# Optimization experiments

Hardware: AMD Instinct MI355X
Metric: run time of the kernel (lower is better)

Reference implementation:

```python
import jax, jax.numpy as jnp
import numpy as np
from jax import lax

PAD_IDX = 0  # padding_index from init
B, T, E, H, V = 128, 24, 512, 512, 10000


def setup_inputs() -> dict:
    key = jax.random.key(0)
    ks = jax.random.split(key, 10)
    return {
        "images": jax.random.normal(ks[0], (B, H), jnp.float32),
        "captions": jax.random.randint(ks[1], (B, T), 0, V),
        "captions_length": jax.random.randint(ks[2], (B,), 1, T + 1),
        "W_emb": jax.random.normal(ks[3], (V, E), jnp.float32) * 0.02,
        "W_ih": jax.random.normal(ks[4], (4 * H, E), jnp.float32) * 0.02,
        "W_hh": jax.random.normal(ks[5], (4 * H, H), jnp.float32) * 0.02,
        "b_ih": jax.random.normal(ks[6], (4 * H,), jnp.float32) * 0.02,
        "b_hh": jax.random.normal(ks[7], (4 * H,), jnp.float32) * 0.02,
        "W_out": jax.random.normal(ks[8], (V, H), jnp.float32) * 0.02,
        "b_out": jax.random.normal(ks[9], (V,), jnp.float32) * 0.02,
    }


def reference(images, captions, captions_length, W_emb, W_ih, W_hh, b_ih, b_hh, W_out, b_out):
    # embedding with padding_idx: padding row forced to zero
    emb_table = W_emb.at[PAD_IDX].set(0.0)
    x = emb_table[captions]  # [B, T, E]
    bdim = images.shape[0]
    hdim = W_hh.shape[1]
    vocab = W_out.shape[0]
    bias = b_ih + b_hh

    def step(carry, xt):
        h, c = carry
        # PyTorch LSTMCell gate order: i, f, g, o
        gates = xt @ W_ih.T + h @ W_hh.T + bias  # [B, 4H]
        i, f, g, o = jnp.split(gates, 4, axis=-1)
        c = jax.nn.sigmoid(f) * c + jax.nn.sigmoid(i) * jnp.tanh(g)
        h = jax.nn.sigmoid(o) * jnp.tanh(c)
        logits = h @ W_out.T + b_out  # [B, V]
        return (h, c), logits

    c0 = jnp.zeros((bdim, hdim), images.dtype)
    _, ys = lax.scan(step, (images, c0), jnp.transpose(x, (1, 0, 2)))  # ys: [T, B, V]

    # deterministic <SOS>-like start output: one-hot at index 1, prepended at t=0
    start = jnp.zeros((vocab,), images.dtype).at[1].set(1.0)
    outputs = jnp.concatenate(
        [jnp.broadcast_to(start, (bdim, 1, vocab)), jnp.transpose(ys, (1, 0, 2))], axis=1
    )  # [B, T+1, V]
    return outputs, captions_length - 1
```

## Files before the change

### kernel.cpp

```cpp
#include <hip/hip_runtime.h>

constexpr int B_  = 128;
constexpr int T_  = 24;
constexpr int E_  = 512;
constexpr int H_  = 512;
constexpr int V_  = 10000;
constexpr int G4  = 2048;
constexpr int TP1 = 25;

typedef __attribute__((ext_vector_type(8))) short bf16x8;
typedef __attribute__((ext_vector_type(4))) short short4v;
typedef __attribute__((ext_vector_type(4))) float f32x4;

#define MFMA_16x16x32_BF16(a, b, c) __builtin_amdgcn_mfma_f32_16x16x32_bf16((a), (b), (c), 0, 0, 0)

__device__ inline unsigned short f2bf(float f) {
    unsigned int u = __float_as_uint(f);
    unsigned int r = (u + 0x7FFFu + ((u >> 16) & 1u)) >> 16;
    return (unsigned short)r;
}

__device__ inline void gl16(const unsigned short* g, unsigned short* l) {
    __builtin_amdgcn_global_load_lds(
        (const __attribute__((address_space(1))) unsigned int*)g,
        (__attribute__((address_space(3))) unsigned int*)l, 16, 0, 0);
}

__device__ inline int swz16(int row, int lq) {
    return (((row << 2) | lq) ^ (row & 7)) << 3;
}

__global__ __launch_bounds__(256) void k_cvt_all(const float* __restrict__ Wih,
                                                 const float* __restrict__ Whh,
                                                 const float* __restrict__ Wout,
                                                 const float* __restrict__ images,
                                                 unsigned short* __restrict__ dWih,
                                                 unsigned short* __restrict__ dWhh,
                                                 unsigned short* __restrict__ dWout,
                                                 unsigned short* __restrict__ dimg,
                                                 unsigned* __restrict__ flg) {
    int b = blockIdx.x;
    if (b == 0) flg[threadIdx.x * 32] = 0u;
    const float* src; unsigned short* dst; int i;
    if (b < 1024)      { src = Wih;    dst = dWih;  i = b * 256 + threadIdx.x; }
    else if (b < 2048) { src = Whh;    dst = dWhh;  i = (b - 1024) * 256 + threadIdx.x; }
    else if (b < 7048) { src = Wout;   dst = dWout; i = (b - 2048) * 256 + threadIdx.x; }
    else               { src = images; dst = dimg;  i = (b - 7048) * 256 + threadIdx.x; }
    float4 v = ((const float4*)src)[i];
    short4v o;
    o[0] = (short)f2bf(v.x); o[1] = (short)f2bf(v.y);
    o[2] = (short)f2bf(v.z); o[3] = (short)f2bf(v.w);
    ((short4v*)dst)[i] = o;
}

__global__ __launch_bounds__(256) void k_embed(const float* __restrict__ Wemb,
                                               const int* __restrict__ captions,
                                               unsigned short* __restrict__ Xemb) {
    int i = blockIdx.x * 256 + threadIdx.x;
    if (i >= 3072 * 128) return;
    int row = i >> 7;
    int k4  = i & 127;
    int b = row & 127, t = row >> 7;
    int tok = captions[b * T_ + t];
    short4v o = {0, 0, 0, 0};
    if (tok > 0 && tok < V_) {
        float4 v = ((const float4*)(Wemb + (long)tok * E_))[k4];
        o[0] = (short)f2bf(v.x); o[1] = (short)f2bf(v.y);
        o[2] = (short)f2bf(v.z); o[3] = (short)f2bf(v.w);
    }
    ((short4v*)Xemb)[(long)row * 128 + k4] = o;
}

__global__ __launch_bounds__(256) void k_start(float* __restrict__ out,
                                               const int* __restrict__ cap_len) {
    int idx = blockIdx.x * 256 + threadIdx.x;
    constexpr int Q = V_ / 4;
    if (idx < B_ * Q) {
        int b = idx / Q;
        int q = idx - b * Q;
        float4 zero = {0.f, 0.f, 0.f, 0.f};
        float4 one1 = {0.f, 1.f, 0.f, 0.f};
        ((float4*)out)[(long)b * (TP1 * Q) + q] = (q == 0) ? one1 : zero;
    }
    if (idx < B_) {
        out[(size_t)B_ * TP1 * V_ + idx] = (float)(cap_len[idx] - 1);
    }
}

__global__ __launch_bounds__(256) void k_pregemm(const unsigned short* __restrict__ Xemb,
                                                 const unsigned short* __restrict__ Wih,
                                                 const float* __restrict__ bih,
                                                 const float* __restrict__ bhh,
                                                 float* __restrict__ P) {
    __shared__ unsigned short ldsA[2][4096];
    __shared__ unsigned short ldsB[2][4096];
    int bid = blockIdx.x;
    int xcd = bid & 7;
    int q   = bid >> 3;
    int MI  = xcd * 3 + (q % 3);
    int NI  = q / 3;
    int i    = threadIdx.x;
    int w = i >> 6, lane = i & 63;
    int lm = lane & 15, lq = lane >> 4;
    int wr = w >> 1, wc = w & 1;

    int mm0 = ((i >> 2) & 7) ^ ((i >> 4) & 1);
    int li  = i ^ mm0;
    const unsigned short* gA = Xemb + (size_t)(MI * 128 + (li >> 2)) * 512 + (li & 3) * 8;
    const unsigned short* gB = Wih  + (size_t)(NI * 128 + (li >> 2)) * 512 + (li & 3) * 8;
    unsigned short* lA = &ldsA[0][0] + i * 8;
    unsigned short* lB = &ldsB[0][0] + i * 8;

    auto stage = [&](int buf, int ks) {
        int go = ks * 32;
        gl16(gA + go,            lA + buf * 4096);
        gl16(gA + go + 64 * 512, lA + buf * 4096 + 2048);
        gl16(gB + go,            lB + buf * 4096);
        gl16(gB + go + 64 * 512, lB + buf * 4096 + 2048);
    };

    f32x4 acc[4][4] = {};
    stage(0, 0);
    for (int ksi = 0; ksi < 16; ksi++) {
        int cur = ksi & 1;
        if (ksi < 15) stage(cur ^ 1, ksi + 1);
        __syncthreads();
        bf16x8 af[4], bfr[4];
        #pragma unroll
        for (int mi = 0; mi < 4; mi++)
            af[mi] = *(const bf16x8*)&ldsA[cur][swz16(wr * 64 + mi * 16 + lm, lq)];
        #pragma unroll
        for (int ni = 0; ni < 4; ni++)
            bfr[ni] = *(const bf16x8*)&ldsB[cur][swz16(wc * 64 + ni * 16 + lm, lq)];
        #pragma unroll
        for (int mi = 0; mi < 4; mi++)
            #pragma unroll
            for (int ni = 0; ni < 4; ni++)
                acc[mi][ni] = MFMA_16x16x32_BF16(af[mi], bfr[ni], acc[mi][ni]);
        __syncthreads();
    }

    float bias[4];
    #pragma unroll
    for (int ni = 0; ni < 4; ni++) {
        int n = NI * 128 + wc * 64 + ni * 16 + lm;
        bias[ni] = bih[n] + bhh[n];
    }
    #pragma unroll
    for (int mi = 0; mi < 4; mi++) {
        #pragma unroll
        for (int r = 0; r < 4; r++) {
            int m = MI * 128 + wr * 64 + mi * 16 + lq * 4 + r;
            #pragma unroll
            for (int ni = 0; ni < 4; ni++) {
                int n = NI * 128 + wc * 64 + ni * 16 + lm;
                P[(size_t)m * G4 + n] = acc[mi][ni][r] + bias[ni];
            }
        }
    }
}

__global__ __launch_bounds__(256, 1) void k_lstm(const float* __restrict__ P,
                                                 const unsigned short* __restrict__ h0,
                                                 unsigned* __restrict__ hx0,
                                                 unsigned* __restrict__ hx1,
                                                 unsigned short* __restrict__ Hall,
                                                 const unsigned short* __restrict__ Whh,
                                                 unsigned* __restrict__ flg) {
    __shared__ float part[16][4][64];
    int w    = threadIdx.x >> 6;
    int lane = threadIdx.x & 63;
    int lm = lane & 15, lq = lane >> 4;
    int MI = blockIdx.x >> 5;
    int HG = blockIdx.x & 31;
    int hcol = HG * 16 + lm;
    int ks = w * 128;
    int brow = MI * 16 + lq * 4 + w;
    unsigned* myFlg = flg + (MI * 32 + HG) * 32;
    unsigned* wFlg  = flg + (MI * 32 + (w << 3)) * 32;

    bf16x8 bw[4][4];
    #pragma unroll
    for (int g = 0; g < 4; g++)
        #pragma unroll
        for (int kk = 0; kk < 4; kk++)
            bw[g][kk] = *(const bf16x8*)((const short*)Whh +
                          (size_t)(g * 512 + hcol) * 512 + ks + kk * 32 + lq * 8);

    float cp = 0.f;

    for (int t = 0; t < T_; t++) {
        const float* Pr = P + (size_t)t * B_ * G4 + (size_t)brow * G4;
        float pv0 = Pr[0 * 512 + hcol];
        float pv1 = Pr[1 * 512 + hcol];
        float pv2 = Pr[2 * 512 + hcol];
        float pv3 = Pr[3 * 512 + hcol];

        bf16x8 a[4];
        if (t == 0) {
            const unsigned short* A = h0 + (size_t)(MI * 16 + lm) * 512 + ks;
            #pragma unroll
            for (int kk = 0; kk < 4; kk++)
                a[kk] = *(const bf16x8*)(A + kk * 32 + lq * 8);
        } else {
            if (lane < 8) {
                unsigned want = (unsigned)t;
                while (__hip_atomic_load(wFlg + lane * 32, __ATOMIC_RELAXED,
                                         __HIP_MEMORY_SCOPE_AGENT) < want)
                    __builtin_amdgcn_s_sleep(1);
            }
            __builtin_amdgcn_wave_barrier();
            asm volatile("" ::: "memory");
            const unsigned long long* A = (const unsigned long long*)
                (((t & 1) ? hx1 : hx0) + ((size_t)(MI * 16 + lm) * 512 + ks) / 2);
            #pragma unroll
            for (int kk = 0; kk < 4; kk++) {
                union { unsigned long long q[2]; bf16x8 v; } cv;
                cv.q[0] = __hip_atomic_load(A + kk * 8 + lq * 2,
                                            __ATOMIC_RELAXED, __HIP_MEMORY_SCOPE_AGENT);
                cv.q[1] = __hip_atomic_load(A + kk * 8 + lq * 2 + 1,
                                            __ATOMIC_RELAXED, __HIP_MEMORY_SCOPE_AGENT);
                a[kk] = cv.v;
            }
        }

        f32x4 acc[4] = {};
        #pragma unroll
        for (int kk = 0; kk < 4; kk++) {
            acc[0] = MFMA_16x16x32_BF16(a[kk], bw[0][kk], acc[0]);
            acc[1] = MFMA_16x16x32_BF16(a[kk], bw[1][kk], acc[1]);
            acc[2] = MFMA_16x16x32_BF16(a[kk], bw[2][kk], acc[2]);
            acc[3] = MFMA_16x16x32_BF16(a[kk], bw[3][kk], acc[3]);
        }

        #pragma unroll
        for (int g = 0; g < 4; g++)
            #pragma unroll
            for (int r = 0; r < 4; r++)
                part[g * 4 + r][w][lane] = acc[g][r];
        __syncthreads();

        float gi = part[0*4+w][0][lane] + part[0*4+w][1][lane] + part[0*4+w][2][lane] + part[0*4+w][3][lane] + pv0;
        float gf = part[1*4+w][0][lane] + part[1*4+w][1][lane] + part[1*4+w][2][lane] + part[1*4+w][3][lane] + pv1;
        float gg = part[2*4+w][0][lane] + part[2*4+w][1][lane] + part[2*4+w][2][lane] + part[2*4+w][3][lane] + pv2;
        float go = part[3*4+w][0][lane] + part[3*4+w][1][lane] + part[3*4+w][2][lane] + part[3*4+w][3][lane] + pv3;
        float si = 1.f / (1.f + expf(-gi));
        float sf = 1.f / (1.f + expf(-gf));
        float so = 1.f / (1.f + expf(-go));
        float cn = sf * cp + si * tanhf(gg);
        float hn = so * tanhf(cn);
        cp = cn;
        unsigned short hb = f2bf(hn);
        Hall[(size_t)t * (B_ * H_) + brow * 512 + hcol] = hb;

        if (t < T_ - 1) {
            unsigned up = ((unsigned)(unsigned short)__shfl_down((int)hb, 1) << 16) | (unsigned)hb;
            unsigned* HW = (t & 1) ? hx0 : hx1;
            if (!(lm & 1))
                __hip_atomic_store(HW + (brow * 512 + hcol) / 2, up,
                                   __ATOMIC_RELAXED, __HIP_MEMORY_SCOPE_AGENT);
            asm volatile("s_waitcnt vmcnt(0)" ::: "memory");
            __syncthreads();
            if (threadIdx.x == 0)
                __hip_atomic_store(myFlg, (unsigned)(t + 1), __ATOMIC_RELAXED,
                                   __HIP_MEMORY_SCOPE_AGENT);
        }
    }
}

__global__ __launch_bounds__(512) void k_logits(const unsigned short* __restrict__ Hall,
                                                const unsigned short* __restrict__ Wout,
                                                const float* __restrict__ bout,
                                                float* __restrict__ out) {
    __shared__ unsigned short ldsA[2][4096];
    __shared__ unsigned short ldsB[2][8192];
    int bid = blockIdx.x;
    int xcd = bid & 7;
    int q   = bid >> 3;
    int MI  = xcd * 3 + (q % 3);
    int NI  = q / 3;
    int i    = threadIdx.x;
    int w = i >> 6, lane = i & 63;
    int lm = lane & 15, lq = lane >> 4;
    int wr = w >> 2, wc = w & 3;

    int mm0 = ((i >> 2) & 7) ^ ((i >> 4) & 1);
    int li  = i ^ mm0;
    const unsigned short* gA = Hall + (size_t)(MI * 128 + (li >> 2)) * 512 + (li & 3) * 8;
    const unsigned short* gB = Wout + (size_t)(NI * 256 + (li >> 2)) * 512 + (li & 3) * 8;
    unsigned short* lA = &ldsA[0][0] + i * 8;
    unsigned short* lB = &ldsB[0][0] + i * 8;

    auto stage = [&](int buf, int ks) {
        int go = ks * 32;
        gl16(gA + go,             lA + buf * 4096);
        gl16(gB + go,             lB + buf * 8192);
        gl16(gB + go + 128 * 512, lB + buf * 8192 + 4096);
    };

    f32x4 acc[4][4] = {};
    stage(0, 0);
    for (int ksi = 0; ksi < 16; ksi++) {
        int cur = ksi & 1;
        if (ksi < 15) stage(cur ^ 1, ksi + 1);
        __syncthreads();
        bf16x8 af[4], bfr[4];
        #pragma unroll
        for (int mi = 0; mi < 4; mi++)
            af[mi] = *(const bf16x8*)&ldsA[cur][swz16(wr * 64 + mi * 16 + lm, lq)];
        #pragma unroll
        for (int ni = 0; ni < 4; ni++)
            bfr[ni] = *(const bf16x8*)&ldsB[cur][swz16(wc * 64 + ni * 16 + lm, lq)];
        #pragma unroll
        for (int mi = 0; mi < 4; mi++)
            #pragma unroll
            for (int ni = 0; ni < 4; ni++)
                acc[mi][ni] = MFMA_16x16x32_BF16(af[mi], bfr[ni], acc[mi][ni]);
        __syncthreads();
    }

    #pragma unroll
    for (int mi = 0; mi < 4; mi++) {
        #pragma unroll
        for (int r = 0; r < 4; r++) {
            int b = wr * 64 + mi * 16 + lq * 4 + r;
            float* orow = out + ((size_t)b * TP1 + MI + 1) * V_;
            #pragma unroll
            for (int ni = 0; ni < 4; ni++) {
                int n = NI * 256 + wc * 64 + ni * 16 + lm;
                if (n < V_) orow[n] = acc[mi][ni][r] + bout[n];
            }
        }
    }
}

extern "C" void kernel_launch(void* const* d_in, const int* in_sizes, int n_in,
                              void* d_out, int out_size, void* d_ws, size_t ws_size,
                              hipStream_t stream) {
    const float* images   = (const float*)d_in[0];
    const int*   captions = (const int*)d_in[1];
    const int*   cap_len  = (const int*)d_in[2];
    const float* Wemb     = (const float*)d_in[3];
    const float* Wih      = (const float*)d_in[4];
    const float* Whh      = (const float*)d_in[5];
    const float* bih      = (const float*)d_in[6];
    const float* bhh      = (const float*)d_in[7];
    const float* Wout     = (const float*)d_in[8];
    const float* bout     = (const float*)d_in[9];
    float* out = (float*)d_out;

    char* ws = (char*)d_ws;
    unsigned short* Wih_bf  = (unsigned short*)(ws);
    unsigned short* Whh_bf  = (unsigned short*)(ws + 2097152);
    unsigned short* Wout_bf = (unsigned short*)(ws + 4194304);
    unsigned short* Xemb    = (unsigned short*)(ws + 14680064);
    unsigned short* Hall    = (unsigned short*)(ws + 17825792);
    unsigned short* h0      = (unsigned short*)(ws + 20971520);
    unsigned*       hx0     = (unsigned*)(ws + 21102592);
    unsigned*       hx1     = (unsigned*)(ws + 21233664);
    unsigned*       flg     = (unsigned*)(ws + 21364736);
    constexpr size_t P_OFF   = 21397504;
    constexpr size_t WS_NEED = P_OFF + 25165824;
    bool ws_ok = (ws_size >= WS_NEED);
    float* P = ws_ok ? (float*)(ws + P_OFF) : (float*)d_out;

    k_cvt_all<<<7112, 256, 0, stream>>>(Wih, Whh, Wout, images,
                                        Wih_bf, Whh_bf, Wout_bf, h0, flg);
    k_embed<<<1536, 256, 0, stream>>>(Wemb, captions, Xemb);

    k_pregemm<<<384, 256, 0, stream>>>(Xemb, Wih_bf, bih, bhh, P);

    if (ws_ok) k_start<<<1250, 256, 0, stream>>>(out, cap_len);

    k_lstm<<<256, 256, 0, stream>>>(P, h0, hx0, hx1, Hall, Whh_bf, flg);

    if (!ws_ok) k_start<<<1250, 256, 0, stream>>>(out, cap_len);

    k_logits<<<960, 512, 0, stream>>>(Hall, Wout_bf, bout, out);
}
```

Measured before the change: 320.0 us.

## Fuse prep kernels, enlarge logits M tile, defer Hall store in LSTM

Merges the weight conversion, embedding gather and start-row writes into one launch, which removes two kernel launches and their gaps. The logits GEMM tile grows from 128x256 to 256x256, halving the grid and raising B-operand reuse. Blocks are remapped so each XCD shares a group of W_out columns. The LSTM now writes its bf16 hidden state to Hall after the flag publish rather than before, taking that store off the cross-block critical path. The larger tile doubles accumulator registers and LDS use, which may lower occupancy.

```diff
diff --git a/kernel.cpp b/kernel.cpp
--- a/kernel.cpp
+++ b/kernel.cpp
@@ -30,45 +30,60 @@
     return (((row << 2) | lq) ^ (row & 7)) << 3;
 }
 
-__global__ __launch_bounds__(256) void k_cvt_all(const float* __restrict__ Wih,
-                                                 const float* __restrict__ Whh,
-                                                 const float* __restrict__ Wout,
-                                                 const float* __restrict__ images,
-                                                 unsigned short* __restrict__ dWih,
-                                                 unsigned short* __restrict__ dWhh,
-                                                 unsigned short* __restrict__ dWout,
-                                                 unsigned short* __restrict__ dimg,
-                                                 unsigned* __restrict__ flg) {
+__global__ __launch_bounds__(256) void k_prep(const float* __restrict__ Wih,
+                                              const float* __restrict__ Whh,
+                                              const float* __restrict__ Wout,
+                                              const float* __restrict__ images,
+                                              const float* __restrict__ Wemb,
+                                              const int* __restrict__ captions,
+                                              const int* __restrict__ cap_len,
+                                              unsigned short* __restrict__ dWih,
+                                              unsigned short* __restrict__ dWhh,
+                                              unsigned short* __restrict__ dWout,
+                                              unsigned short* __restrict__ dimg,
+                                              unsigned short* __restrict__ Xemb,
+                                              float* __restrict__ out,
+                                              unsigned* __restrict__ flg,
+                                              int do_start) {
     int b = blockIdx.x;
     if (b == 0) flg[threadIdx.x * 32] = 0u;
-    const float* src; unsigned short* dst; int i;
-    if (b < 1024)      { src = Wih;    dst = dWih;  i = b * 256 + threadIdx.x; }
-    else if (b < 2048) { src = Whh;    dst = dWhh;  i = (b - 1024) * 256 + threadIdx.x; }
-    else if (b < 7048) { src = Wout;   dst = dWout; i = (b - 2048) * 256 + threadIdx.x; }
-    else               { src = images; dst = dimg;  i = (b - 7048) * 256 + threadIdx.x; }
-    float4 v = ((const float4*)src)[i];
-    short4v o;
-    o[0] = (short)f2bf(v.x); o[1] = (short)f2bf(v.y);
-    o[2] = (short)f2bf(v.z); o[3] = (short)f2bf(v.w);
-    ((short4v*)dst)[i] = o;
-}
-
-__global__ __launch_bounds__(256) void k_embed(const float* __restrict__ Wemb,
-                                               const int* __restrict__ captions,
-                                               unsigned short* __restrict__ Xemb) {
-    int i = blockIdx.x * 256 + threadIdx.x;
-    if (i >= 3072 * 128) return;
-    int row = i >> 7;
-    int k4  = i & 127;
-    int b = row & 127, t = row >> 7;
-    int tok = captions[b * T_ + t];
-    short4v o = {0, 0, 0, 0};
-    if (tok > 0 && tok < V_) {
-        float4 v = ((const float4*)(Wemb + (long)tok * E_))[k4];
+    if (b < 7112) {
+        const float* src; unsigned short* dst; int i;
+        if (b < 1024)      { src = Wih;    dst = dWih;  i = b * 256 + threadIdx.x; }
+        else if (b < 2048) { src = Whh;    dst = dWhh;  i = (b - 1024) * 256 + threadIdx.x; }
+        else if (b < 7048) { src = Wout;   dst = dWout; i = (b - 2048) * 256 + threadIdx.x; }
+        else               { src = images; dst = dimg;  i = (b - 7048) * 256 + threadIdx.x; }
+        float4 v = ((const float4*)src)[i];
+        short4v o;
         o[0] = (short)f2bf(v.x); o[1] = (short)f2bf(v.y);
         o[2] = (short)f2bf(v.z); o[3] = (short)f2bf(v.w);
-    }
-    ((short4v*)Xemb)[(long)row * 128 + k4] = o;
+        ((short4v*)dst)[i] = o;
+    } else if (b < 8648) {
+        int i = (b - 7112) * 256 + threadIdx.x;
+        int row = i >> 7;
+        int k4  = i & 127;
+        int bb = row & 127, t = row >> 7;
+        int tok = captions[bb * T_ + t];
+        short4v o = {0, 0, 0, 0};
+        if (tok > 0 && tok < V_) {
+            float4 v = ((const float4*)(Wemb + (long)tok * E_))[k4];
+            o[0] = (short)f2bf(v.x); o[1] = (short)f2bf(v.y);
+            o[2] = (short)f2bf(v.z); o[3] = (short)f2bf(v.w);
+        }
+        ((short4v*)Xemb)[(long)row * 128 + k4] = o;
+    } else if (do_start) {
+        int idx = (b - 8648) * 256 + threadIdx.x;
+        constexpr int Q = V_ / 4;
+        if (idx < B_ * Q) {
+            int bb = idx / Q;
+            int q = idx - bb * Q;
+            float4 zero = {0.f, 0.f, 0.f, 0.f};
+            float4 one1 = {0.f, 1.f, 0.f, 0.f};
+            ((float4*)out)[(long)bb * (TP1 * Q) + q] = (q == 0) ? one1 : zero;
+        }
+        if (idx < B_)
+            out[(size_t)B_ * TP1 * V_ + idx] = (float)(cap_len[idx] - 1);
+    }
 }
 
 __global__ __launch_bounds__(256) void k_start(float* __restrict__ out,
@@ -82,9 +97,7 @@
         float4 one1 = {0.f, 1.f, 0.f, 0.f};
         ((float4*)out)[(long)b * (TP1 * Q) + q] = (q == 0) ? one1 : zero;
     }
-    if (idx < B_) {
-        out[(size_t)B_ * TP1 * V_ + idx] = (float)(cap_len[idx] - 1);
-    }
+    if (idx < B_) out[(size_t)B_ * TP1 * V_ + idx] = (float)(cap_len[idx] - 1);
 }
 
 __global__ __launch_bounds__(256) void k_pregemm(const unsigned short* __restrict__ Xemb,
@@ -251,7 +264,6 @@
         float hn = so * tanhf(cn);
         cp = cn;
         unsigned short hb = f2bf(hn);
-        Hall[(size_t)t * (B_ * H_) + brow * 512 + hcol] = hb;
 
         if (t < T_ - 1) {
             unsigned up = ((unsigned)(unsigned short)__shfl_down((int)hb, 1) << 16) | (unsigned)hb;
@@ -265,6 +277,7 @@
                 __hip_atomic_store(myFlg, (unsigned)(t + 1), __ATOMIC_RELAXED,
                                    __HIP_MEMORY_SCOPE_AGENT);
         }
+        Hall[(size_t)t * (B_ * H_) + brow * 512 + hcol] = hb;
     }
 }
 
@@ -272,13 +285,13 @@
                                                 const unsigned short* __restrict__ Wout,
                                                 const float* __restrict__ bout,
                                                 float* __restrict__ out) {
-    __shared__ unsigned short ldsA[2][4096];
+    __shared__ unsigned short ldsA[2][8192];
     __shared__ unsigned short ldsB[2][8192];
     int bid = blockIdx.x;
     int xcd = bid & 7;
     int q   = bid >> 3;
-    int MI  = xcd * 3 + (q % 3);
-    int NI  = q / 3;
+    int MI  = q % 12;
+    int NI  = xcd * 5 + q / 12;
     int i    = threadIdx.x;
     int w = i >> 6, lane = i & 63;
     int lm = lane & 15, lq = lane >> 4;
@@ -286,49 +299,58 @@
 
     int mm0 = ((i >> 2) & 7) ^ ((i >> 4) & 1);
     int li  = i ^ mm0;
-    const unsigned short* gA = Hall + (size_t)(MI * 128 + (li >> 2)) * 512 + (li & 3) * 8;
+    const unsigned short* gA = Hall + (size_t)(MI * 256 + (li >> 2)) * 512 + (li & 3) * 8;
     const unsigned short* gB = Wout + (size_t)(NI * 256 + (li >> 2)) * 512 + (li & 3) * 8;
     unsigned short* lA = &ldsA[0][0] + i * 8;
     unsigned short* lB = &ldsB[0][0] + i * 8;
 
     auto stage = [&](int buf, int ks) {
         int go = ks * 32;
-        gl16(gA + go,             lA + buf * 4096);
+        gl16(gA + go,             lA + buf * 8192);
+        gl16(gA + go + 128 * 512, lA + buf * 8192 + 4096);
         gl16(gB + go,             lB + buf * 8192);
         gl16(gB + go + 128 * 512, lB + buf * 8192 + 4096);
     };
 
-    f32x4 acc[4][4] = {};
+    f32x4 acc[8][4] = {};
     stage(0, 0);
     for (int ksi = 0; ksi < 16; ksi++) {
         int cur = ksi & 1;
         if (ksi < 15) stage(cur ^ 1, ksi + 1);
         __syncthreads();
-        bf16x8 af[4], bfr[4];
-        #pragma unroll
-        for (int mi = 0; mi < 4; mi++)
-            af[mi] = *(const bf16x8*)&ldsA[cur][swz16(wr * 64 + mi * 16 + lm, lq)];
+        bf16x8 af[8], bfr[4];
+        #pragma unroll
+        for (int mi = 0; mi < 8; mi++)
+            af[mi] = *(const bf16x8*)&ldsA[cur][swz16(wr * 128 + mi * 16 + lm, lq)];
         #pragma unroll
         for (int ni = 0; ni < 4; ni++)
             bfr[ni] = *(const bf16x8*)&ldsB[cur][swz16(wc * 64 + ni * 16 + lm, lq)];
         #pragma unroll
-        for (int mi = 0; mi < 4; mi++)
+        for (int mi = 0; mi < 8; mi++)
             #pragma unroll
             for (int ni = 0; ni < 4; ni++)
                 acc[mi][ni] = MFMA_16x16x32_BF16(af[mi], bfr[ni], acc[mi][ni]);
         __syncthreads();
     }
 
+    float bias[4];
     #pragma unroll
-    for (int mi = 0; mi < 4; mi++) {
+    for (int ni = 0; ni < 4; ni++) {
+        int n = NI * 256 + wc * 64 + ni * 16 + lm;
+        bias[ni] = (n < V_) ? bout[n] : 0.f;
+    }
+
+    #pragma unroll
+    for (int mi = 0; mi < 8; mi++) {
         #pragma unroll
         for (int r = 0; r < 4; r++) {
-            int b = wr * 64 + mi * 16 + lq * 4 + r;
-            float* orow = out + ((size_t)b * TP1 + MI + 1) * V_;
+            int m = MI * 256 + wr * 128 + mi * 16 + lq * 4 + r;
+            int b = m & 127, t = m >> 7;
+            float* orow = out + ((size_t)b * TP1 + t + 1) * V_;
             #pragma unroll
             for (int ni = 0; ni < 4; ni++) {
                 int n = NI * 256 + wc * 64 + ni * 16 + lm;
-                if (n < V_) orow[n] = acc[mi][ni][r] + bout[n];
+                if (n < V_) orow[n] = acc[mi][ni][r] + bias[ni];
             }
         }
     }
@@ -364,17 +386,15 @@
     bool ws_ok = (ws_size >= WS_NEED);
     float* P = ws_ok ? (float*)(ws + P_OFF) : (float*)d_out;
 
-    k_cvt_all<<<7112, 256, 0, stream>>>(Wih, Whh, Wout, images,
-                                        Wih_bf, Whh_bf, Wout_bf, h0, flg);
-    k_embed<<<1536, 256, 0, stream>>>(Wemb, captions, Xemb);
+    k_prep<<<9898, 256, 0, stream>>>(Wih, Whh, Wout, images, Wemb, captions,
+                                     cap_len, Wih_bf, Whh_bf, Wout_bf, h0,
+                                     Xemb, out, flg, ws_ok ? 1 : 0);
 
     k_pregemm<<<384, 256, 0, stream>>>(Xemb, Wih_bf, bih, bhh, P);
 
-    if (ws_ok) k_start<<<1250, 256, 0, stream>>>(out, cap_len);
-
     k_lstm<<<256, 256, 0, stream>>>(P, h0, hx0, hx1, Hall, Whh_bf, flg);
 
     if (!ws_ok) k_start<<<1250, 256, 0, stream>>>(out, cap_len);
 
-    k_logits<<<960, 512, 0, stream>>>(Hall, Wout_bf, bout, out);
-}
+    k_logits<<<480, 512, 0, stream>>>(Hall, Wout_bf, bout, out);
+}
```

Measured after the change: 330.2 us. 3.2% more time.
